# Kernel tuning notes

Hardware: AMD Instinct MI355X
Metric: run time of the kernel (lower is better)

## Reference

```python
import jax, jax.numpy as jnp
import numpy as np

S, R, CM, CZ, H = 128, 256, 256, 128, 8
HD = CM // H
INF = 1e9
EPS = 1e-5


def _ln(x, g, b):
    mu = jnp.mean(x, axis=-1, keepdims=True)
    var = jnp.var(x, axis=-1, keepdims=True)
    return (x - mu) * jax.lax.rsqrt(var + EPS) * g + b


def setup_inputs() -> dict:
    key = jax.random.key(0)
    ks = jax.random.split(key, 12)
    d = {
        'm': jax.random.normal(ks[0], (S, R, CM), jnp.float32),
        'z': jax.random.normal(ks[1], (R, R, CZ), jnp.float32),
        'mask': jnp.ones((S, R), jnp.float32),
        'ln_m_g': jnp.ones((CM,), jnp.float32),
        'ln_m_b': jnp.zeros((CM,), jnp.float32),
        'ln_z_g': jnp.ones((CZ,), jnp.float32),
        'ln_z_b': jnp.zeros((CZ,), jnp.float32),
        'w_z': jax.random.normal(ks[2], (CZ, H), jnp.float32) * 0.02,
        'wq': jax.random.normal(ks[3], (CM, CM), jnp.float32) * (1.0 / np.sqrt(CM)),
        'wk': jax.random.normal(ks[4], (CM, CM), jnp.float32) * (1.0 / np.sqrt(CM)),
        'wv': jax.random.normal(ks[5], (CM, CM), jnp.float32) * (1.0 / np.sqrt(CM)),
        'wg': jnp.zeros((CM, CM), jnp.float32),
        'bg': jnp.ones((CM,), jnp.float32),
        'wo': jax.random.normal(ks[6], (CM, CM), jnp.float32) * (1.0 / np.sqrt(CM)),
        'bo': jnp.zeros((CM,), jnp.float32),
    }
    return d


def reference(m, z, mask, ln_m_g, ln_m_b, ln_z_g, ln_z_b, w_z, wq, wk, wv, wg, bg, wo, bo):
    # pair bias: LN(z) -> per-head bias [H, R, R], broadcast over seq rows
    z_ln = _ln(z, ln_z_g, ln_z_b)
    pair_bias = jnp.einsum('ijc,ch->hij', z_ln, w_z)          # [H, R, R]
    mask_bias = (INF * (mask - 1.0))[:, None, None, :]        # [S, 1, 1, R]

    m_ln = _ln(m, ln_m_g, ln_m_b)                             # [S, R, CM]
    q = (m_ln @ wq).reshape(S, R, H, HD)
    k = (m_ln @ wk).reshape(S, R, H, HD)
    v = (m_ln @ wv).reshape(S, R, H, HD)

    scale = 1.0 / np.sqrt(HD).astype(np.float32)
    logits = jnp.einsum('sihd,sjhd->shij', q * scale, k)       # [S, H, R, R]
    logits = logits + pair_bias[None] + mask_bias
    attn = jax.nn.softmax(logits, axis=-1)

    o = jnp.einsum('shij,sjhd->sihd', attn, v).reshape(S, R, CM)
    g = jax.nn.sigmoid(m_ln @ wg + bg)
    return (g * o) @ wo + bo
```

## Files before the change

### kernel.cpp

```cpp
#include <hip/hip_runtime.h>
#include <hip/hip_bf16.h>

typedef unsigned short u16;
typedef __bf16 bf16x8 __attribute__((ext_vector_type(8)));
typedef float f32x4 __attribute__((ext_vector_type(4)));
typedef float f32x16 __attribute__((ext_vector_type(16)));
typedef unsigned short u16x8 __attribute__((ext_vector_type(8)));
typedef unsigned short u16x4 __attribute__((ext_vector_type(4)));

#define LOG2E 1.4426950408889634f

__device__ __forceinline__ u16 f2b(float f) {
  union { __bf16 b; u16 u; } v; v.b = (__bf16)f; return v.u;
}
__device__ __forceinline__ float bf2f(u16 u) {
  union { unsigned u; float f; } v; v.u = ((unsigned)u) << 16;
  return v.f;
}
__device__ __forceinline__ float fexp2(float x) {
  return __builtin_amdgcn_exp2f(x);
}

__global__ __launch_bounds__(256) void k_pre(
    const float* __restrict__ wq, const float* __restrict__ wk,
    const float* __restrict__ wv, const float* __restrict__ wg,
    const float* __restrict__ wo, u16* __restrict__ wtp,
    const float* __restrict__ z, const float* __restrict__ zg,
    const float* __restrict__ zb, const float* __restrict__ wz,
    float* __restrict__ pbp,
    const float* __restrict__ m, const float* __restrict__ gam,
    const float* __restrict__ bet, u16* __restrict__ mlp) {
  __shared__ float lt[64][68];
  const int b = blockIdx.x;
  const int t = threadIdx.x;
  if (b < 80) {
    const int widx = b >> 4;
    const int tid = b & 15;
    const int ri = (tid >> 2) * 64, ci = (tid & 3) * 64;
    const float* src = (widx == 0) ? wq : (widx == 1) ? wk : (widx == 2) ? wv
                      : (widx == 3) ? wg : wo;
    {
      const int r = t >> 2;
      #pragma unroll
      for (int i = 0; i < 4; ++i) {
        const int c = (t & 3) * 16 + i * 4;
        *(float4*)&lt[r][c] = *(const float4*)&src[(ri + r) * 256 + ci + c];
      }
    }
    __syncthreads();
    #pragma unroll
    for (int cc = 0; cc < 2; ++cc) {
      const int c = t + cc * 256;
      const int kb = c >> 8, cb = (c >> 6) & 3, lg = (c >> 4) & 3, lr = c & 15;
      u16x8 o;
      #pragma unroll
      for (int j = 0; j < 8; ++j) o[j] = f2b(lt[kb * 32 + lg * 8 + j][cb * 16 + lr]);
      const size_t idx = (size_t)widx * 65536 + (size_t)((ci >> 4) + cb) * 4096
                       + (size_t)((ri >> 5) + kb) * 512 + (size_t)(lg * 16 + lr) * 8;
      *(u16x8*)&wtp[idx] = o;
    }
  } else if (b < 4176) {
    const int lane = t & 63, wave = t >> 6;
    const int ql = lane & 15;
    const int p = (b - 80) * 16 + wave * 4 + (lane >> 4);
    const float4 zv0 = *(const float4*)(z + (size_t)p * 128 + ql * 8);
    const float4 zv1 = *(const float4*)(z + (size_t)p * 128 + ql * 8 + 4);
    float s = zv0.x + zv0.y + zv0.z + zv0.w + zv1.x + zv1.y + zv1.z + zv1.w;
    float sq = zv0.x * zv0.x + zv0.y * zv0.y + zv0.z * zv0.z + zv0.w * zv0.w
             + zv1.x * zv1.x + zv1.y * zv1.y + zv1.z * zv1.z + zv1.w * zv1.w;
    #pragma unroll
    for (int o = 8; o > 0; o >>= 1) { s += __shfl_xor(s, o); sq += __shfl_xor(sq, o); }
    const float mu = s * 0.0078125f;
    const float var = sq * 0.0078125f - mu * mu;
    const float rs = rsqrtf(var + 1e-5f);
    const int c0 = ql * 8;
    float zn[8];
    zn[0] = (zv0.x - mu) * rs * zg[c0 + 0] + zb[c0 + 0];
    zn[1] = (zv0.y - mu) * rs * zg[c0 + 1] + zb[c0 + 1];
    zn[2] = (zv0.z - mu) * rs * zg[c0 + 2] + zb[c0 + 2];
    zn[3] = (zv0.w - mu) * rs * zg[c0 + 3] + zb[c0 + 3];
    zn[4] = (zv1.x - mu) * rs * zg[c0 + 4] + zb[c0 + 4];
    zn[5] = (zv1.y - mu) * rs * zg[c0 + 5] + zb[c0 + 5];
    zn[6] = (zv1.z - mu) * rs * zg[c0 + 6] + zb[c0 + 6];
    zn[7] = (zv1.w - mu) * rs * zg[c0 + 7] + zb[c0 + 7];
    float a[8] = {};
    #pragma unroll
    for (int i = 0; i < 8; ++i) {
      #pragma unroll
      for (int hh = 0; hh < 8; ++hh) a[hh] += zn[i] * wz[(c0 + i) * 8 + hh];
    }
    #pragma unroll
    for (int hh = 0; hh < 8; ++hh) {
      #pragma unroll
      for (int o = 8; o > 0; o >>= 1) a[hh] += __shfl_xor(a[hh], o);
    }
    if (ql == 0) {
      const int i = p >> 8, j = p & 255;
      const int strip = i >> 5, il = i & 31, jt = j >> 5, r = j & 31;
      const int gh = (r >> 2) & 1, qd = r >> 3, c4 = r & 3;
      const int off = (strip * 8 + jt) * 1024 + (gh * 32 + il) * 16 + qd * 4 + c4;
      #pragma unroll
      for (int hh = 0; hh < 8; ++hh)
        pbp[(size_t)hh * 65536 + off] = a[hh] * LOG2E;
    }
  } else {
    const int lane = t & 63;
    const size_t row = (size_t)(b - 4176) * 4 + (t >> 6);
    const float4 xv = *(const float4*)(m + row * 256 + lane * 4);
    float s = xv.x + xv.y + xv.z + xv.w;
    float sq = xv.x * xv.x + xv.y * xv.y + xv.z * xv.z + xv.w * xv.w;
    #pragma unroll
    for (int o = 32; o > 0; o >>= 1) { s += __shfl_xor(s, o); sq += __shfl_xor(sq, o); }
    const float mu = s * 0.00390625f;
    const float var = sq * 0.00390625f - mu * mu;
    const float rs = rsqrtf(var + 1e-5f);
    const int c = lane * 4;
    u16x4 o4;
    o4.x = f2b((xv.x - mu) * rs * gam[c] + bet[c]);
    o4.y = f2b((xv.y - mu) * rs * gam[c + 1] + bet[c + 1]);
    o4.z = f2b((xv.z - mu) * rs * gam[c + 2] + bet[c + 2]);
    o4.w = f2b((xv.w - mu) * rs * gam[c + 3] + bet[c + 3]);
    const size_t ss = row >> 8;
    const int rloc = (int)(row & 255);
    const int ch = rloc >> 5, il = rloc & 31;
    const size_t dst = ss * 65536 + (size_t)ch * 8192 + (size_t)(lane >> 2) * 512
                     + (size_t)(((lane >> 1) & 1) * 32 + il) * 8 + (lane & 1) * 4;
    *(u16x4*)&mlp[dst] = o4;
  }
}

__global__ __launch_bounds__(512, 4) void k_fused(
    const u16* __restrict__ mlp, const u16* __restrict__ wtp,
    const float* __restrict__ bg, const float* __restrict__ pbp,
    const float* __restrict__ mask, u16* __restrict__ go) {
  __shared__ u16 gP[256 * 32];
  __shared__ u16 lQ[256 * 32];
  __shared__ u16 lK[256 * 32];
  __shared__ u16 lVt[32][276];
  __shared__ float lMb[256];
  __shared__ float lL[8][32];
  const int bid = blockIdx.x;
  const int s = bid & 127, h = bid >> 7;
  const int t = threadIdx.x;
  const int lane = t & 63, wave = t >> 6;
  const int il = lane & 31, gh = lane >> 5;
  const int z = wave >> 1, half = wave & 1;

  const u16* Wb = wtp + (size_t)z * 65536 + (size_t)(2 * h + (il >> 4)) * 4096
                + gh * 128 + (il & 15) * 8;
  bf16x8 B[16];
  #pragma unroll
  for (int kc = 0; kc < 16; ++kc) B[kc] = *(const bf16x8*)&Wb[kc * 256];

  if (t < 256)
    lMb[t] = (LOG2E * 1e9f) * (mask[s * 256 + t] - 1.0f) - 24.0f;
  const float bgv = bg[h * 32 + il];
  const u16* Ab = mlp + (size_t)s * 65536 + (size_t)lane * 8;

  #pragma unroll
  for (int cc = 0; cc < 4; ++cc) {
    const int c = half * 4 + cc;
    f32x16 a0 = {}, a1 = {};
    bf16x8 A0[8];
    #pragma unroll
    for (int kc = 0; kc < 8; ++kc)
      A0[kc] = *(const bf16x8*)&Ab[c * 8192 + kc * 512];
    #pragma unroll
    for (int kc = 0; kc < 8; kc += 2) {
      a0 = __builtin_amdgcn_mfma_f32_32x32x16_bf16(A0[kc], B[kc], a0, 0, 0, 0);
      a1 = __builtin_amdgcn_mfma_f32_32x32x16_bf16(A0[kc + 1], B[kc + 1], a1, 0, 0, 0);
    }
    bf16x8 A1[8];
    #pragma unroll
    for (int kc = 0; kc < 8; ++kc)
      A1[kc] = *(const bf16x8*)&Ab[c * 8192 + (kc + 8) * 512];
    #pragma unroll
    for (int kc = 0; kc < 8; kc += 2) {
      a0 = __builtin_amdgcn_mfma_f32_32x32x16_bf16(A1[kc], B[kc + 8], a0, 0, 0, 0);
      a1 = __builtin_amdgcn_mfma_f32_32x32x16_bf16(A1[kc + 1], B[kc + 9], a1, 0, 0, 0);
    }
    const f32x16 acc = a0 + a1;
    if (z == 0) {
      #pragma unroll
      for (int reg = 0; reg < 16; ++reg) {
        const int R = c * 32 + (reg & 3) + 8 * (reg >> 2) + 4 * gh;
        *(u16*)((char*)lQ + ((R * 64 + il * 2) ^ ((R & 7) << 4))) =
            f2b(acc[reg] * (0.17677669529663687f * LOG2E));
      }
    } else if (z == 1) {
      #pragma unroll
      for (int reg = 0; reg < 16; ++reg) {
        const int R = c * 32 + (reg & 3) + 8 * (reg >> 2) + 4 * gh;
        *(u16*)((char*)lK + ((R * 64 + il * 2) ^ ((R & 7) << 4))) = f2b(acc[reg]);
      }
    } else if (z == 2) {
      #pragma unroll
      for (int reg = 0; reg < 16; ++reg) {
        const int R = c * 32 + (reg & 3) + 8 * (reg >> 2) + 4 * gh;
        lVt[il][R] = f2b(acc[reg]);
      }
    } else {
      #pragma unroll
      for (int reg = 0; reg < 16; ++reg) {
        const int R = c * 32 + (reg & 3) + 8 * (reg >> 2) + 4 * gh;
        const float x = acc[reg] + bgv;
        gP[R * 32 + il] = f2b(1.0f / (1.0f + __expf(-x)));
      }
    }
  }
  __syncthreads();

  {
    const int i0 = wave * 32;
    bf16x8 qf[2];
    #pragma unroll
    for (int kk = 0; kk < 2; ++kk) {
      const int row = i0 + il;
      qf[kk] = *(const bf16x8*)((const char*)lQ +
          ((row * 64 + (kk * 16 + gh * 8) * 2) ^ ((row & 7) << 4)));
    }
    const float* pbt = pbp + ((size_t)h * 8 + wave) * 8192 + lane * 16;

    f32x16 oacc0 = {}, oacc1 = {};
    float s0 = 0.f, s1 = 0.f, s2 = 0.f, s3 = 0.f;

    #pragma unroll 2
    for (int jt = 0; jt < 8; ++jt) {
      const float* pl = pbt + jt * 1024;
      f32x16 c;
      #pragma unroll
      for (int qd = 0; qd < 4; ++qd) {
        const f32x4 pbq = *(const f32x4*)&pl[qd * 4];
        const f32x4 mb4 = *(const f32x4*)&lMb[jt * 32 + qd * 8 + gh * 4];
        #pragma unroll
        for (int c4 = 0; c4 < 4; ++c4)
          c[qd * 4 + c4] = pbq[c4] + mb4[c4];
      }
      const int krow = jt * 32 + il;
      const bf16x8 kf0 = *(const bf16x8*)((const char*)lK +
          ((krow * 64 + (gh * 8) * 2) ^ ((krow & 7) << 4)));
      const bf16x8 kf1 = *(const bf16x8*)((const char*)lK +
          ((krow * 64 + (16 + gh * 8) * 2) ^ ((krow & 7) << 4)));
      c = __builtin_amdgcn_mfma_f32_32x32x16_bf16(kf0, qf[0], c, 0, 0, 0);
      c = __builtin_amdgcn_mfma_f32_32x32x16_bf16(kf1, qf[1], c, 0, 0, 0);
      union PK { __bf16 h[4]; uint2 u; } pk[4];
      #pragma unroll
      for (int qd = 0; qd < 4; ++qd) {
        const float p0 = fexp2(c[qd * 4 + 0]);
        const float p1 = fexp2(c[qd * 4 + 1]);
        const float p2 = fexp2(c[qd * 4 + 2]);
        const float p3 = fexp2(c[qd * 4 + 3]);
        s0 += p0; s1 += p1; s2 += p2; s3 += p3;
        pk[qd].h[0] = (__bf16)p0; pk[qd].h[1] = (__bf16)p1;
        pk[qd].h[2] = (__bf16)p2; pk[qd].h[3] = (__bf16)p3;
      }
      const uint2 sA = gh ? pk[0].u : pk[1].u;
      uint2 rA; rA.x = __shfl_xor(sA.x, 32); rA.y = __shfl_xor(sA.y, 32);
      const uint2 sB = gh ? pk[2].u : pk[3].u;
      uint2 rB; rB.x = __shfl_xor(sB.x, 32); rB.y = __shfl_xor(sB.y, 32);
      union FR { uint2 u2[2]; bf16x8 v; } fa0, fa1;
      fa0.u2[0] = gh ? rA : pk[0].u;
      fa0.u2[1] = gh ? pk[1].u : rA;
      fa1.u2[0] = gh ? rB : pk[2].u;
      fa1.u2[1] = gh ? pk[3].u : rB;
      const bf16x8 vf0 = *(const bf16x8*)&lVt[il][jt * 32 + gh * 8];
      const bf16x8 vf1 = *(const bf16x8*)&lVt[il][jt * 32 + 16 + gh * 8];
      oacc0 = __builtin_amdgcn_mfma_f32_32x32x16_bf16(fa0.v, vf0, oacc0, 0, 0, 0);
      oacc1 = __builtin_amdgcn_mfma_f32_32x32x16_bf16(fa1.v, vf1, oacc1, 0, 0, 0);
    }

    float lsum = (s0 + s1) + (s2 + s3);
    lsum += __shfl_xor(lsum, 32);
    if (lane < 32) lL[wave][il] = 1.0f / lsum;

    #pragma unroll
    for (int qd = 0; qd < 4; ++qd) {
      const f32x4 invq = *(const f32x4*)&lL[wave][qd * 8 + gh * 4];
      #pragma unroll
      for (int c4 = 0; c4 < 4; ++c4) {
        const int iloc = qd * 8 + gh * 4 + c4;
        const size_t row = (size_t)s * 256 + i0 + iloc;
        const int col = h * 32 + il;
        const float ov = (oacc0[qd * 4 + c4] + oacc1[qd * 4 + c4]) * invq[c4];
        const float gv = bf2f(gP[(i0 + iloc) * 32 + il]);
        go[row * 256 + col] = f2b(gv * ov);
      }
    }
  }
}

__global__ __launch_bounds__(256, 4) void k_gemm_out(
    const u16* __restrict__ go, const u16* __restrict__ wop,
    const float* __restrict__ bo, float* __restrict__ out) {
  __shared__ u16 lA[32 * 256];
  const int t = threadIdx.x;
  const size_t row0 = (size_t)blockIdx.x * 32;
  const int lane = t & 63, wave = t >> 6;
  const u16* Wz = wop + (size_t)wave * 16384 + (size_t)lane * 8;
  u16x8 areg[4];
  #pragma unroll
  for (int i = 0; i < 4; ++i)
    areg[i] = *(const u16x8*)&go[(row0 + i * 8 + (t >> 5)) * 256 + (t & 31) * 8];
  bf16x8 B[4][4];
  #pragma unroll
  for (int kc = 0; kc < 4; ++kc) {
    #pragma unroll
    for (int nn = 0; nn < 4; ++nn)
      B[kc][nn] = *(const bf16x8*)&Wz[nn * 4096 + kc * 512];
  }
  __builtin_amdgcn_sched_barrier(0);
  #pragma unroll
  for (int i = 0; i < 4; ++i) {
    const int r = i * 8 + (t >> 5);
    const int c = (t & 31) * 8;
    *(u16x8*)((char*)lA + ((r * 512 + c * 2) ^ ((r & 7) << 4))) = areg[i];
  }
  __syncthreads();
  const int lrow = lane & 15, lg = lane >> 4;
  f32x4 acc[2][4] = {};
  #pragma unroll
  for (int kc = 0; kc < 4; ++kc) {
    bf16x8 af[2];
    #pragma unroll
    for (int mm = 0; mm < 2; ++mm) {
      const int row = mm * 16 + lrow;
      af[mm] = *(const bf16x8*)((const char*)lA +
          ((row * 512 + kc * 64 + lg * 16) ^ ((row & 7) << 4)));
    }
    #pragma unroll
    for (int mm = 0; mm < 2; ++mm) {
      #pragma unroll
      for (int nn = 0; nn < 4; ++nn)
        acc[mm][nn] = __builtin_amdgcn_mfma_f32_16x16x32_bf16(
            af[mm], B[kc][nn], acc[mm][nn], 0, 0, 0);
    }
  }
  #pragma unroll
  for (int kc = 0; kc < 4; ++kc) {
    #pragma unroll
    for (int nn = 0; nn < 4; ++nn)
      B[kc][nn] = *(const bf16x8*)&Wz[nn * 4096 + (kc + 4) * 512];
  }
  __builtin_amdgcn_sched_barrier(0);
  #pragma unroll
  for (int kc = 0; kc < 4; ++kc) {
    bf16x8 af[2];
    #pragma unroll
    for (int mm = 0; mm < 2; ++mm) {
      const int row = mm * 16 + lrow;
      af[mm] = *(const bf16x8*)((const char*)lA +
          ((row * 512 + (kc + 4) * 64 + lg * 16) ^ ((row & 7) << 4)));
    }
    #pragma unroll
    for (int mm = 0; mm < 2; ++mm) {
      #pragma unroll
      for (int nn = 0; nn < 4; ++nn)
        acc[mm][nn] = __builtin_amdgcn_mfma_f32_16x16x32_bf16(
            af[mm], B[kc][nn], acc[mm][nn], 0, 0, 0);
    }
  }
  const int wc = wave * 64, lg4 = lg * 4;
  #pragma unroll
  for (int mm = 0; mm < 2; ++mm) {
    #pragma unroll
    for (int nn = 0; nn < 4; ++nn) {
      const int col = wc + nn * 16 + lrow;
      #pragma unroll
      for (int jr = 0; jr < 4; ++jr) {
        const size_t row = row0 + mm * 16 + lg4 + jr;
        out[row * 256 + col] = acc[mm][nn][jr] + bo[col];
      }
    }
  }
}

extern "C" void kernel_launch(void* const* d_in, const int* in_sizes, int n_in,
                              void* d_out, int out_size, void* d_ws, size_t ws_size,
                              hipStream_t stream) {
  const float* m      = (const float*)d_in[0];
  const float* z      = (const float*)d_in[1];
  const float* mask   = (const float*)d_in[2];
  const float* ln_m_g = (const float*)d_in[3];
  const float* ln_m_b = (const float*)d_in[4];
  const float* ln_z_g = (const float*)d_in[5];
  const float* ln_z_b = (const float*)d_in[6];
  const float* w_z    = (const float*)d_in[7];
  const float* wq     = (const float*)d_in[8];
  const float* wk     = (const float*)d_in[9];
  const float* wv     = (const float*)d_in[10];
  const float* wg     = (const float*)d_in[11];
  const float* bg     = (const float*)d_in[12];
  const float* wo     = (const float*)d_in[13];
  const float* bo     = (const float*)d_in[14];
  float* out = (float*)d_out;

  char* w = (char*)d_ws;
  u16* wtp   = (u16*)w;   w += (size_t)5 * 65536 * 2;
  float* pbp = (float*)w; w += (size_t)8 * 65536 * 4;
  u16* mlp   = (u16*)w;   w += (size_t)32768 * 256 * 2;
  u16* gow   = (u16*)w;   w += (size_t)32768 * 256 * 2;

  k_pre      <<<12368, 256, 0, stream>>>(wq, wk, wv, wg, wo, wtp,
                                         z, ln_z_g, ln_z_b, w_z, pbp,
                                         m, ln_m_g, ln_m_b, mlp);
  k_fused    <<<1024, 512, 0, stream>>>(mlp, wtp, bg, pbp, mask, gow);
  k_gemm_out <<<1024, 256, 0, stream>>>(gow, wtp + (size_t)4 * 65536, bo, out);
}
```

Baseline: 113.1 us.

## Prefetch pair-bias tiles, raise wave priority around MFMAs, reorder block-to-head mapping

The attention loop now loads the next iteration's pair-bias tile from global memory into registers while the current tile is being processed, and is fully unrolled, so the load latency overlaps the MFMA and exp work. MFMA groups are wrapped with s_setprio so waves issuing matrix ops get scheduling priority over waves doing loads. Block indexing changes to put all heads of one sequence row next to each other, which may improve L2 reuse of that row's activations. Together these raise register pressure under launch bounds of 4 blocks per SM, and the priority hints may do nothing.

```diff
diff --git a/kernel.cpp b/kernel.cpp
--- a/kernel.cpp
+++ b/kernel.cpp
@@ -140,7 +140,7 @@
   __shared__ float lMb[256];
   __shared__ float lL[8][32];
   const int bid = blockIdx.x;
-  const int s = bid & 127, h = bid >> 7;
+  const int h = bid & 7, s = bid >> 3;
   const int t = threadIdx.x;
   const int lane = t & 63, wave = t >> 6;
   const int il = lane & 31, gh = lane >> 5;
@@ -165,20 +165,24 @@
     #pragma unroll
     for (int kc = 0; kc < 8; ++kc)
       A0[kc] = *(const bf16x8*)&Ab[c * 8192 + kc * 512];
+    __builtin_amdgcn_s_setprio(1);
     #pragma unroll
     for (int kc = 0; kc < 8; kc += 2) {
       a0 = __builtin_amdgcn_mfma_f32_32x32x16_bf16(A0[kc], B[kc], a0, 0, 0, 0);
       a1 = __builtin_amdgcn_mfma_f32_32x32x16_bf16(A0[kc + 1], B[kc + 1], a1, 0, 0, 0);
     }
+    __builtin_amdgcn_s_setprio(0);
     bf16x8 A1[8];
     #pragma unroll
     for (int kc = 0; kc < 8; ++kc)
       A1[kc] = *(const bf16x8*)&Ab[c * 8192 + (kc + 8) * 512];
+    __builtin_amdgcn_s_setprio(1);
     #pragma unroll
     for (int kc = 0; kc < 8; kc += 2) {
       a0 = __builtin_amdgcn_mfma_f32_32x32x16_bf16(A1[kc], B[kc + 8], a0, 0, 0, 0);
       a1 = __builtin_amdgcn_mfma_f32_32x32x16_bf16(A1[kc + 1], B[kc + 9], a1, 0, 0, 0);
     }
+    __builtin_amdgcn_s_setprio(0);
     const f32x16 acc = a0 + a1;
     if (z == 0) {
       #pragma unroll
@@ -224,25 +228,44 @@
     f32x16 oacc0 = {}, oacc1 = {};
     float s0 = 0.f, s1 = 0.f, s2 = 0.f, s3 = 0.f;
 
-    #pragma unroll 2
+    f32x4 pq0 = *(const f32x4*)&pbt[0];
+    f32x4 pq1 = *(const f32x4*)&pbt[4];
+    f32x4 pq2 = *(const f32x4*)&pbt[8];
+    f32x4 pq3 = *(const f32x4*)&pbt[12];
+
+    #pragma unroll
     for (int jt = 0; jt < 8; ++jt) {
-      const float* pl = pbt + jt * 1024;
+      f32x4 pn0, pn1, pn2, pn3;
+      if (jt < 7) {
+        const float* pl = pbt + (jt + 1) * 1024;
+        pn0 = *(const f32x4*)&pl[0];
+        pn1 = *(const f32x4*)&pl[4];
+        pn2 = *(const f32x4*)&pl[8];
+        pn3 = *(const f32x4*)&pl[12];
+      }
       f32x16 c;
-      #pragma unroll
-      for (int qd = 0; qd < 4; ++qd) {
-        const f32x4 pbq = *(const f32x4*)&pl[qd * 4];
-        const f32x4 mb4 = *(const f32x4*)&lMb[jt * 32 + qd * 8 + gh * 4];
+      {
+        const f32x4 mb0 = *(const f32x4*)&lMb[jt * 32 + 0 * 8 + gh * 4];
+        const f32x4 mb1 = *(const f32x4*)&lMb[jt * 32 + 1 * 8 + gh * 4];
+        const f32x4 mb2 = *(const f32x4*)&lMb[jt * 32 + 2 * 8 + gh * 4];
+        const f32x4 mb3 = *(const f32x4*)&lMb[jt * 32 + 3 * 8 + gh * 4];
         #pragma unroll
-        for (int c4 = 0; c4 < 4; ++c4)
-          c[qd * 4 + c4] = pbq[c4] + mb4[c4];
+        for (int c4 = 0; c4 < 4; ++c4) {
+          c[0 * 4 + c4] = pq0[c4] + mb0[c4];
+          c[1 * 4 + c4] = pq1[c4] + mb1[c4];
+          c[2 * 4 + c4] = pq2[c4] + mb2[c4];
+          c[3 * 4 + c4] = pq3[c4] + mb3[c4];
+        }
       }
       const int krow = jt * 32 + il;
       const bf16x8 kf0 = *(const bf16x8*)((const char*)lK +
           ((krow * 64 + (gh * 8) * 2) ^ ((krow & 7) << 4)));
       const bf16x8 kf1 = *(const bf16x8*)((const char*)lK +
           ((krow * 64 + (16 + gh * 8) * 2) ^ ((krow & 7) << 4)));
+      __builtin_amdgcn_s_setprio(1);
       c = __builtin_amdgcn_mfma_f32_32x32x16_bf16(kf0, qf[0], c, 0, 0, 0);
       c = __builtin_amdgcn_mfma_f32_32x32x16_bf16(kf1, qf[1], c, 0, 0, 0);
+      __builtin_amdgcn_s_setprio(0);
       union PK { __bf16 h[4]; uint2 u; } pk[4];
       #pragma unroll
       for (int qd = 0; qd < 4; ++qd) {
@@ -265,8 +288,11 @@
       fa1.u2[1] = gh ? pk[3].u : rB;
       const bf16x8 vf0 = *(const bf16x8*)&lVt[il][jt * 32 + gh * 8];
       const bf16x8 vf1 = *(const bf16x8*)&lVt[il][jt * 32 + 16 + gh * 8];
+      __builtin_amdgcn_s_setprio(1);
       oacc0 = __builtin_amdgcn_mfma_f32_32x32x16_bf16(fa0.v, vf0, oacc0, 0, 0, 0);
       oacc1 = __builtin_amdgcn_mfma_f32_32x32x16_bf16(fa1.v, vf1, oacc1, 0, 0, 0);
+      __builtin_amdgcn_s_setprio(0);
+      if (jt < 7) { pq0 = pn0; pq1 = pn1; pq2 = pn2; pq3 = pn3; }
     }
 
     float lsum = (s0 + s1) + (s2 + s3);
```

Result: slower. 160.7 us (+42.1%).
